# Kernel tuning notes

Hardware: AMD Instinct MI355X
Metric: run time of the kernel (lower is better)

The kernel has to match this reference:

```python
import jax, jax.numpy as jnp
import numpy as np

NUM_TABLES = 26
ROWS = 100000
EMB = 64
B = 4096
L = 32  # num_lookups per bag
BOT = [256, 512, 256, 64]
TOP = [EMB * (1 + NUM_TABLES), 512, 256, 1]


def _mlp_params(key, dims):
    params = []
    for i in range(len(dims) - 1):
        din, dout = dims[i], dims[i + 1]
        kw, kb, key = jax.random.split(key, 3)
        sw = np.sqrt(2.0 / (din + dout)).astype(np.float32)
        sb = np.sqrt(1.0 / dout).astype(np.float32)
        params.append((jax.random.normal(kw, (dout, din), jnp.float32) * sw,
                       jax.random.normal(kb, (dout,), jnp.float32) * sb))
    return params


def setup_inputs() -> dict:
    key = jax.random.key(0)
    k0, k1, k2, k3, k4 = jax.random.split(key, 5)
    inp = {}
    inp["x_dense"] = jax.random.normal(k0, (B, BOT[0]), jnp.float32)
    inp["x_indices"] = jax.random.randint(k1, (NUM_TABLES, B, L), 0, ROWS)
    bound = np.sqrt(1.0 / ROWS).astype(np.float32)
    inp["emb_tables"] = jax.random.uniform(k2, (NUM_TABLES, ROWS, EMB), jnp.float32, -bound, bound)
    for i, (w, b) in enumerate(_mlp_params(k3, BOT)):
        inp[f"bot_w{i}"] = w
        inp[f"bot_b{i}"] = b
    for i, (w, b) in enumerate(_mlp_params(k4, TOP)):
        inp[f"top_w{i}"] = w
        inp[f"top_b{i}"] = b
    return inp


def _forward(x_dense, x_indices, emb_tables, bot, top):
    # bottom MLP: Linear+ReLU per layer
    h = x_dense
    for w, b in bot:
        h = jax.nn.relu(h @ w.T + b)
    # multi-table EmbeddingBag(mode='sum'): gather rows then sum over bag dim
    # pooled: [T, B, E]
    pooled = jax.vmap(lambda tbl, idx: jnp.take(tbl, idx, axis=0).sum(axis=1))(emb_tables, x_indices)
    emb = jnp.transpose(pooled, (1, 0, 2)).reshape(x_dense.shape[0], -1)  # [B, T*E]
    z = jnp.concatenate([h, emb], axis=1)  # [B, E*(1+T)]
    # top MLP: ReLU on all but last, sigmoid on last
    n = len(top)
    for i, (w, b) in enumerate(top):
        z = z @ w.T + b
        z = jax.nn.sigmoid(z) if i == n - 1 else jax.nn.relu(z)
    return z


def reference(x_dense, x_indices, emb_tables,
              bot_w0, bot_b0, bot_w1, bot_b1, bot_w2, bot_b2,
              top_w0, top_b0, top_w1, top_b1, top_w2, top_b2):
    bot = [(bot_w0, bot_b0), (bot_w1, bot_b1), (bot_w2, bot_b2)]
    top = [(top_w0, top_b0), (top_w1, top_b1), (top_w2, top_b2)]
    return _forward(x_dense, x_indices, emb_tables, bot, top)
```

## Files before the change

kernel.cpp:

```cpp
#include <hip/hip_runtime.h>
#include <hip/hip_bf16.h>
#include <math.h>

typedef __attribute__((ext_vector_type(8))) short short8;
typedef __attribute__((ext_vector_type(4))) float f32x4;

#define NUM_TABLES 26
#define ROWS 100000
#define EMB 64
#define BATCH 4096
#define LOOKUPS 32
#define ZDIM 1728

#define CAST_BLOCKS 128
#define BOT_BLOCKS 256
#define EMBED_BLOCKS (NUM_TABLES * BATCH / 4)

__device__ __forceinline__ unsigned short f2bf(float f) {
  unsigned int u = __float_as_uint(f);
  u += 0x7FFFu + ((u >> 16) & 1u);
  return (unsigned short)(u >> 16);
}
__device__ __forceinline__ float bf2f(unsigned short h) {
  return __uint_as_float(((unsigned int)h) << 16);
}

__device__ __forceinline__ void gload16(const void* g, void* l) {
  __builtin_amdgcn_global_load_lds(
      (const __attribute__((address_space(1))) void*)g,
      (__attribute__((address_space(3))) void*)l, 16, 0, 0);
}

__device__ __forceinline__ short8 wfrag_f32(const float* __restrict__ W, int K,
                                            int colbase, int l, int kc) {
  const float* p = W + (size_t)(colbase + (l & 15)) * K + kc * 32 + ((l >> 4) << 3);
  float4 u = *(const float4*)p;
  float4 v = *(const float4*)(p + 4);
  short8 f;
  f[0] = (short)f2bf(u.x); f[1] = (short)f2bf(u.y);
  f[2] = (short)f2bf(u.z); f[3] = (short)f2bf(u.w);
  f[4] = (short)f2bf(v.x); f[5] = (short)f2bf(v.y);
  f[6] = (short)f2bf(v.z); f[7] = (short)f2bf(v.w);
  return f;
}

struct MegaArgs {
  const float* cast_s[2];
  unsigned short* cast_d[2];
  int cast_n4[2];
  int cast_total;
  const float* x_dense;
  const float* bw0; const float* bb0;
  const float* bw1; const float* bb1;
  const float* bw2; const float* bb2;
  const int* idx;
  const float* tables;
  unsigned short* z;
};

__global__ void mega(MegaArgs a) {
  __shared__ unsigned short xb[16][256];
  __shared__ unsigned short h0[16][512];

  if (blockIdx.x < CAST_BLOCKS) {
    for (int i = blockIdx.x * blockDim.x + threadIdx.x; i < a.cast_total;
         i += CAST_BLOCKS * blockDim.x) {
      int r = i;
      #pragma unroll
      for (int sg = 0; sg < 2; ++sg) {
        if (r < a.cast_n4[sg]) {
          float4 v = ((const float4*)a.cast_s[sg])[r];
          ushort4 o;
          o.x = f2bf(v.x); o.y = f2bf(v.y); o.z = f2bf(v.z); o.w = f2bf(v.w);
          ((ushort4*)a.cast_d[sg])[r] = o;
          break;
        }
        r -= a.cast_n4[sg];
      }
    }
    return;
  }

  if (blockIdx.x < CAST_BLOCKS + BOT_BLOCKS) {
    int b0 = (int)(blockIdx.x - CAST_BLOCKS) << 4;
    int w = threadIdx.x >> 6;
    int l = threadIdx.x & 63;

    #pragma unroll
    for (int i = 0; i < 4; ++i) {
      int flat = i * 256 + threadIdx.x;
      int row = flat >> 6;
      int c4 = flat & 63;
      float4 v = *(const float4*)(a.x_dense + (size_t)(b0 + row) * 256 + c4 * 4);
      int chunk = c4 >> 1;
      int scol = ((chunk ^ (row & 7)) << 3) | ((c4 & 1) << 2);
      ushort4 o;
      o.x = f2bf(v.x); o.y = f2bf(v.y); o.z = f2bf(v.z); o.w = f2bf(v.w);
      *(ushort4*)&xb[row][scol] = o;
    }
    __syncthreads();

    int arow = l & 15;
    int sA = arow & 7;
    const char* xbp = (const char*)&xb[0][0];
    const char* h0p = (const char*)&h0[0][0];

    f32x4 acc0[8];
    #pragma unroll
    for (int n = 0; n < 8; ++n) acc0[n] = (f32x4){0.f, 0.f, 0.f, 0.f};
    for (int kc = 0; kc < 8; ++kc) {
      int c = kc * 4 + (l >> 4);
      short8 av = *(const short8*)(xbp + arow * 512 + ((c ^ sA) << 4));
      #pragma unroll
      for (int n = 0; n < 8; ++n) {
        short8 bv = wfrag_f32(a.bw0, 256, w * 128 + n * 16, l, kc);
        acc0[n] = __builtin_amdgcn_mfma_f32_16x16x32_bf16(av, bv, acc0[n], 0, 0, 0);
      }
    }
    #pragma unroll
    for (int n = 0; n < 8; ++n) {
      int col = w * 128 + n * 16 + (l & 15);
      float bv = a.bb0[col];
      int chunk = col >> 3;
      #pragma unroll
      for (int r = 0; r < 4; ++r) {
        int row = ((l >> 4) << 2) + r;
        float val = acc0[n][r] + bv;
        val = val > 0.f ? val : 0.f;
        h0[row][((chunk ^ (row & 7)) << 3) | (col & 7)] = f2bf(val);
      }
    }
    __syncthreads();

    f32x4 acc1[4];
    #pragma unroll
    for (int n = 0; n < 4; ++n) acc1[n] = (f32x4){0.f, 0.f, 0.f, 0.f};
    for (int kc = 0; kc < 16; ++kc) {
      int c = kc * 4 + (l >> 4);
      short8 av = *(const short8*)(h0p + arow * 1024 + ((c ^ sA) << 4));
      #pragma unroll
      for (int n = 0; n < 4; ++n) {
        short8 bv = wfrag_f32(a.bw1, 512, w * 64 + n * 16, l, kc);
        acc1[n] = __builtin_amdgcn_mfma_f32_16x16x32_bf16(av, bv, acc1[n], 0, 0, 0);
      }
    }
    __syncthreads();
    #pragma unroll
    for (int n = 0; n < 4; ++n) {
      int col = w * 64 + n * 16 + (l & 15);
      float bv = a.bb1[col];
      int chunk = col >> 3;
      #pragma unroll
      for (int r = 0; r < 4; ++r) {
        int row = ((l >> 4) << 2) + r;
        float val = acc1[n][r] + bv;
        val = val > 0.f ? val : 0.f;
        xb[row][((chunk ^ (row & 7)) << 3) | (col & 7)] = f2bf(val);
      }
    }
    __syncthreads();

    f32x4 acc2 = (f32x4){0.f, 0.f, 0.f, 0.f};
    for (int kc = 0; kc < 8; ++kc) {
      int c = kc * 4 + (l >> 4);
      short8 av = *(const short8*)(xbp + arow * 512 + ((c ^ sA) << 4));
      short8 bv = wfrag_f32(a.bw2, 256, w * 16, l, kc);
      acc2 = __builtin_amdgcn_mfma_f32_16x16x32_bf16(av, bv, acc2, 0, 0, 0);
    }
    {
      int col = w * 16 + (l & 15);
      float bv = a.bb2[col];
      #pragma unroll
      for (int r = 0; r < 4; ++r) {
        int row = ((l >> 4) << 2) + r;
        float val = acc2[r] + bv;
        val = val > 0.f ? val : 0.f;
        a.z[(size_t)(b0 + row) * ZDIM + col] = f2bf(val);
      }
    }
    return;
  }

  int g = (int)(((blockIdx.x - CAST_BLOCKS - BOT_BLOCKS) << 2) + (threadIdx.x >> 6));
  int lane = threadIdx.x & 63;
  int t = g >> 12;
  int b = g & 4095;
  const int* ip = a.idx + ((size_t)t * BATCH + b) * LOOKUPS;
  int myidx = (lane < LOOKUPS) ? ip[lane] : 0;
  const float* tbl = a.tables + (size_t)t * ROWS * EMB;
  int grp = lane >> 4;
  int e4 = lane & 15;
  float4 acc = {0.f, 0.f, 0.f, 0.f};
  #pragma unroll
  for (int it = 0; it < 8; ++it) {
    int r = __shfl(myidx, it * 4 + grp, 64);
    float4 v = ((const float4*)(tbl + (size_t)r * EMB))[e4];
    acc.x += v.x; acc.y += v.y; acc.z += v.z; acc.w += v.w;
  }
  #pragma unroll
  for (int m = 16; m <= 32; m <<= 1) {
    acc.x += __shfl_xor(acc.x, m, 64);
    acc.y += __shfl_xor(acc.y, m, 64);
    acc.z += __shfl_xor(acc.z, m, 64);
    acc.w += __shfl_xor(acc.w, m, 64);
  }
  if (lane < 16) {
    ushort4 o;
    o.x = f2bf(acc.x); o.y = f2bf(acc.y); o.z = f2bf(acc.z); o.w = f2bf(acc.w);
    *(ushort4*)&a.z[(size_t)b * ZDIM + EMB + t * EMB + e4 * 4] = o;
  }
}

template<int ACT>
__global__ __launch_bounds__(256) void gemm64s(
    const unsigned short* __restrict__ A,
    const unsigned short* __restrict__ W,
    const float* __restrict__ bias,
    unsigned short* __restrict__ C,
    int M, int N, int K, int ldc) {
  __shared__ unsigned short lds[2][64][64];

  int t = threadIdx.x;
  int lane = t & 63;
  int wid = t >> 6;
  int wr = wid >> 1;
  int wc = wid & 1;

  int bid = (int)blockIdx.x;
  int q = (int)gridDim.x >> 3;
  int swz = (bid & 7) * q + (bid >> 3);

  int ntn = N >> 6;
  int tm = swz / ntn;
  int tn = swz - tm * ntn;

  int srow = lane >> 3;
  int schunk = (lane & 7) ^ (srow & 7);
  const unsigned short* Ap0 = A + (size_t)(tm * 64 + wid * 16 + srow) * K + schunk * 8;
  const unsigned short* Wp0 = W + (size_t)(tn * 64 + wid * 16 + srow) * K + schunk * 8;
  size_t rowK8 = (size_t)8 * K;

  f32x4 acc[2][2];
  #pragma unroll
  for (int m = 0; m < 2; ++m)
    #pragma unroll
    for (int n = 0; n < 2; ++n)
      acc[m][n] = (f32x4){0.f, 0.f, 0.f, 0.f};

  int ra = wr * 32 + (lane & 15);
  int rb = wc * 32 + (lane & 15);
  int cidx = lane >> 4;
  int sA = ra & 7, sB = rb & 7;

  for (int k0 = 0; k0 < K; k0 += 64) {
    #pragma unroll
    for (int j = 0; j < 2; ++j) {
      gload16(Ap0 + (size_t)k0 + j * rowK8, &lds[0][wid * 16 + j * 8][0]);
      gload16(Wp0 + (size_t)k0 + j * rowK8, &lds[1][wid * 16 + j * 8][0]);
    }
    __syncthreads();

    const char* bA = (const char*)&lds[0][0][0];
    const char* bB = (const char*)&lds[1][0][0];
    #pragma unroll
    for (int kc = 0; kc < 2; ++kc) {
      int c = kc * 4 + cidx;
      short8 a0 = *(const short8*)(bA + ra * 128 + ((c ^ sA) << 4));
      short8 a1 = *(const short8*)(bA + (ra + 16) * 128 + ((c ^ sA) << 4));
      short8 b0 = *(const short8*)(bB + rb * 128 + ((c ^ sB) << 4));
      short8 b1 = *(const short8*)(bB + (rb + 16) * 128 + ((c ^ sB) << 4));
      acc[0][0] = __builtin_amdgcn_mfma_f32_16x16x32_bf16(a0, b0, acc[0][0], 0, 0, 0);
      acc[0][1] = __builtin_amdgcn_mfma_f32_16x16x32_bf16(a0, b1, acc[0][1], 0, 0, 0);
      acc[1][0] = __builtin_amdgcn_mfma_f32_16x16x32_bf16(a1, b0, acc[1][0], 0, 0, 0);
      acc[1][1] = __builtin_amdgcn_mfma_f32_16x16x32_bf16(a1, b1, acc[1][1], 0, 0, 0);
    }
    __syncthreads();
  }

  #pragma unroll
  for (int m = 0; m < 2; ++m) {
    int drow = tm * 64 + wr * 32 + m * 16 + ((lane >> 4) << 2);
    #pragma unroll
    for (int n = 0; n < 2; ++n) {
      int dcol = tn * 64 + wc * 32 + n * 16 + (lane & 15);
      float bv = bias[dcol];
      #pragma unroll
      for (int r = 0; r < 4; ++r) {
        float v = acc[m][n][r] + bv;
        if (ACT == 1) v = v > 0.f ? v : 0.f;
        C[(size_t)(drow + r) * ldc + dcol] = f2bf(v);
      }
    }
  }
}

__global__ __launch_bounds__(256) void topfin256(
    const unsigned short* __restrict__ z1,
    const unsigned short* __restrict__ w1,
    const float* __restrict__ b1,
    const float* __restrict__ w2,
    const float* __restrict__ b2,
    float* __restrict__ out) {
  __shared__ float red[4][16];
  int l = threadIdx.x & 63;
  int w = threadIdx.x >> 6;
  int row0 = (int)blockIdx.x * 16;

  f32x4 acc[4];
  #pragma unroll
  for (int n = 0; n < 4; ++n) acc[n] = (f32x4){0.f, 0.f, 0.f, 0.f};

  const unsigned short* ap0 = z1 + (size_t)(row0 + (l & 15)) * 512 + ((l >> 4) << 3);
  const unsigned short* bp0 = w1 + (size_t)(w * 64 + (l & 15)) * 512 + ((l >> 4) << 3);
  #pragma unroll 4
  for (int kc = 0; kc < 16; ++kc) {
    short8 av = *(const short8*)(ap0 + kc * 32);
    #pragma unroll
    for (int n = 0; n < 4; ++n) {
      short8 bv = *(const short8*)(bp0 + (size_t)n * 16 * 512 + kc * 32);
      acc[n] = __builtin_amdgcn_mfma_f32_16x16x32_bf16(av, bv, acc[n], 0, 0, 0);
    }
  }

  float s0 = 0.f, s1 = 0.f, s2 = 0.f, s3 = 0.f;
  #pragma unroll
  for (int n = 0; n < 4; ++n) {
    int col = w * 64 + n * 16 + (l & 15);
    float bv = b1[col];
    float wv = w2[col];
    float v0 = acc[n][0] + bv; v0 = v0 > 0.f ? v0 : 0.f; s0 += v0 * wv;
    float v1 = acc[n][1] + bv; v1 = v1 > 0.f ? v1 : 0.f; s1 += v1 * wv;
    float v2 = acc[n][2] + bv; v2 = v2 > 0.f ? v2 : 0.f; s2 += v2 * wv;
    float v3 = acc[n][3] + bv; v3 = v3 > 0.f ? v3 : 0.f; s3 += v3 * wv;
  }
  #pragma unroll
  for (int m = 1; m <= 8; m <<= 1) {
    s0 += __shfl_xor(s0, m, 64);
    s1 += __shfl_xor(s1, m, 64);
    s2 += __shfl_xor(s2, m, 64);
    s3 += __shfl_xor(s3, m, 64);
  }
  if ((l & 15) == 0) {
    int rbase = (l >> 4) * 4;
    red[w][rbase + 0] = s0;
    red[w][rbase + 1] = s1;
    red[w][rbase + 2] = s2;
    red[w][rbase + 3] = s3;
  }
  __syncthreads();
  if (threadIdx.x < 16) {
    float s = red[0][threadIdx.x] + red[1][threadIdx.x] +
              red[2][threadIdx.x] + red[3][threadIdx.x];
    out[row0 + threadIdx.x] = 1.f / (1.f + expf(-(s + b2[0])));
  }
}

extern "C" void kernel_launch(void* const* d_in, const int* in_sizes, int n_in,
                              void* d_out, int out_size, void* d_ws, size_t ws_size,
                              hipStream_t stream) {
  const float* x_dense = (const float*)d_in[0];
  const int*   x_idx   = (const int*)d_in[1];
  const float* tables  = (const float*)d_in[2];
  const float* bw0 = (const float*)d_in[3];  const float* bb0 = (const float*)d_in[4];
  const float* bw1 = (const float*)d_in[5];  const float* bb1 = (const float*)d_in[6];
  const float* bw2 = (const float*)d_in[7];  const float* bb2 = (const float*)d_in[8];
  const float* tw0 = (const float*)d_in[9];  const float* tb0 = (const float*)d_in[10];
  const float* tw1 = (const float*)d_in[11]; const float* tb1 = (const float*)d_in[12];
  const float* tw2 = (const float*)d_in[13]; const float* tb2 = (const float*)d_in[14];
  float* out = (float*)d_out;

  char* ws = (char*)d_ws;
  size_t off = 0;
  auto alloc = [&](size_t bytes) { void* p = ws + off; off += (bytes + 255) & ~(size_t)255; return p; };
  unsigned short* tw0b = (unsigned short*)alloc((size_t)512 * ZDIM * 2);
  unsigned short* tw1b = (unsigned short*)alloc((size_t)256 * 512 * 2);
  unsigned short* z    = (unsigned short*)alloc((size_t)BATCH * ZDIM * 2);
  unsigned short* z1   = (unsigned short*)alloc((size_t)BATCH * 512 * 2);

  {
    MegaArgs a;
    a.cast_s[0] = tw0; a.cast_d[0] = tw0b; a.cast_n4[0] = 512 * ZDIM / 4;
    a.cast_s[1] = tw1; a.cast_d[1] = tw1b; a.cast_n4[1] = 256 * 512 / 4;
    a.cast_total = a.cast_n4[0] + a.cast_n4[1];
    a.x_dense = x_dense;
    a.bw0 = bw0; a.bb0 = bb0;
    a.bw1 = bw1; a.bb1 = bb1;
    a.bw2 = bw2; a.bb2 = bb2;
    a.idx = x_idx;
    a.tables = tables;
    a.z = z;
    mega<<<CAST_BLOCKS + BOT_BLOCKS + EMBED_BLOCKS, 256, 0, stream>>>(a);
  }

  gemm64s<1><<<512, 256, 0, stream>>>(z, tw0b, tb0, z1, BATCH, 512, ZDIM, 512);

  topfin256<<<BATCH / 16, 256, 0, stream>>>(z1, tw1b, tb1, tw2, tb2, out);
}
```

Before: 174.9 us.

## Split-K the top-layer-0 GEMM three ways and fuse the reduction into the final kernel

The 4096x512x1728 GEMM now runs as a 3-way split-K over 1536 blocks instead of 512, so more CUs stay busy. Each split writes fp32 partial sums to a workspace. The final kernel sums the three partials, adds bias and ReLU, converts to bf16 and stages the result in swizzled LDS before its MFMA loop. In exchange it writes and reads about 24 MB of fp32 partials instead of a 4 MB bf16 intermediate.

```diff
diff --git a/kernel.cpp b/kernel.cpp
--- a/kernel.cpp
+++ b/kernel.cpp
@@ -211,13 +211,10 @@
   }
 }
 
-template<int ACT>
-__global__ __launch_bounds__(256) void gemm64s(
+__global__ __launch_bounds__(256) void gemm_top0_sk(
     const unsigned short* __restrict__ A,
     const unsigned short* __restrict__ W,
-    const float* __restrict__ bias,
-    unsigned short* __restrict__ C,
-    int M, int N, int K, int ldc) {
+    float* __restrict__ z1p) {
   __shared__ unsigned short lds[2][64][64];
 
   int t = threadIdx.x;
@@ -227,18 +224,18 @@
   int wc = wid & 1;
 
   int bid = (int)blockIdx.x;
-  int q = (int)gridDim.x >> 3;
-  int swz = (bid & 7) * q + (bid >> 3);
-
-  int ntn = N >> 6;
-  int tm = swz / ntn;
-  int tn = swz - tm * ntn;
+  int swz = (bid & 7) * 192 + (bid >> 3);
+  int kh = swz / 512;
+  int tid = swz - kh * 512;
+  int tm = tid >> 3;
+  int tn = tid & 7;
+  int kstart = kh * 576;
 
   int srow = lane >> 3;
   int schunk = (lane & 7) ^ (srow & 7);
-  const unsigned short* Ap0 = A + (size_t)(tm * 64 + wid * 16 + srow) * K + schunk * 8;
-  const unsigned short* Wp0 = W + (size_t)(tn * 64 + wid * 16 + srow) * K + schunk * 8;
-  size_t rowK8 = (size_t)8 * K;
+  const unsigned short* Ap0 = A + (size_t)(tm * 64 + wid * 16 + srow) * ZDIM + schunk * 8;
+  const unsigned short* Wp0 = W + (size_t)(tn * 64 + wid * 16 + srow) * ZDIM + schunk * 8;
+  size_t rowK8 = (size_t)8 * ZDIM;
 
   f32x4 acc[2][2];
   #pragma unroll
@@ -252,7 +249,8 @@
   int cidx = lane >> 4;
   int sA = ra & 7, sB = rb & 7;
 
-  for (int k0 = 0; k0 < K; k0 += 64) {
+  for (int s = 0; s < 9; ++s) {
+    int k0 = kstart + s * 64;
     #pragma unroll
     for (int j = 0; j < 2; ++j) {
       gload16(Ap0 + (size_t)k0 + j * rowK8, &lds[0][wid * 16 + j * 8][0]);
@@ -277,44 +275,72 @@
     __syncthreads();
   }
 
+  float* Cp = z1p + (size_t)kh * BATCH * 512;
   #pragma unroll
   for (int m = 0; m < 2; ++m) {
     int drow = tm * 64 + wr * 32 + m * 16 + ((lane >> 4) << 2);
     #pragma unroll
     for (int n = 0; n < 2; ++n) {
       int dcol = tn * 64 + wc * 32 + n * 16 + (lane & 15);
-      float bv = bias[dcol];
-      #pragma unroll
-      for (int r = 0; r < 4; ++r) {
-        float v = acc[m][n][r] + bv;
-        if (ACT == 1) v = v > 0.f ? v : 0.f;
-        C[(size_t)(drow + r) * ldc + dcol] = f2bf(v);
-      }
+      #pragma unroll
+      for (int r = 0; r < 4; ++r)
+        Cp[(size_t)(drow + r) * 512 + dcol] = acc[m][n][r];
     }
   }
 }
 
 __global__ __launch_bounds__(256) void topfin256(
-    const unsigned short* __restrict__ z1,
+    const float* __restrict__ z1p,
+    const float* __restrict__ tb0,
     const unsigned short* __restrict__ w1,
-    const float* __restrict__ b1,
+    const float* __restrict__ tb1,
     const float* __restrict__ w2,
     const float* __restrict__ b2,
     float* __restrict__ out) {
+  __shared__ unsigned short zb[16][512];
   __shared__ float red[4][16];
   int l = threadIdx.x & 63;
   int w = threadIdx.x >> 6;
   int row0 = (int)blockIdx.x * 16;
 
+  const float* p0 = z1p;
+  const float* p1 = z1p + (size_t)BATCH * 512;
+  const float* p2 = z1p + (size_t)2 * BATCH * 512;
+
+  #pragma unroll
+  for (int i = 0; i < 8; ++i) {
+    int idx4 = i * 256 + threadIdx.x;
+    int row = idx4 >> 7;
+    int col = (idx4 & 127) * 4;
+    size_t gi = (size_t)(row0 + row) * 512 + col;
+    float4 v0 = *(const float4*)(p0 + gi);
+    float4 v1 = *(const float4*)(p1 + gi);
+    float4 v2 = *(const float4*)(p2 + gi);
+    float4 bb = *(const float4*)(tb0 + col);
+    float e0 = v0.x + v1.x + v2.x + bb.x; e0 = e0 > 0.f ? e0 : 0.f;
+    float e1 = v0.y + v1.y + v2.y + bb.y; e1 = e1 > 0.f ? e1 : 0.f;
+    float e2 = v0.z + v1.z + v2.z + bb.z; e2 = e2 > 0.f ? e2 : 0.f;
+    float e3 = v0.w + v1.w + v2.w + bb.w; e3 = e3 > 0.f ? e3 : 0.f;
+    ushort4 o;
+    o.x = f2bf(e0); o.y = f2bf(e1); o.z = f2bf(e2); o.w = f2bf(e3);
+    int chunk = col >> 3;
+    int scol = ((chunk ^ (row & 7)) << 3) | (col & 7);
+    *(ushort4*)&zb[row][scol] = o;
+  }
+  __syncthreads();
+
   f32x4 acc[4];
   #pragma unroll
   for (int n = 0; n < 4; ++n) acc[n] = (f32x4){0.f, 0.f, 0.f, 0.f};
 
-  const unsigned short* ap0 = z1 + (size_t)(row0 + (l & 15)) * 512 + ((l >> 4) << 3);
+  const char* zbp = (const char*)&zb[0][0];
+  int arow = l & 15;
+  int sA = arow & 7;
   const unsigned short* bp0 = w1 + (size_t)(w * 64 + (l & 15)) * 512 + ((l >> 4) << 3);
   #pragma unroll 4
   for (int kc = 0; kc < 16; ++kc) {
-    short8 av = *(const short8*)(ap0 + kc * 32);
+    int c = kc * 4 + (l >> 4);
+    short8 av = *(const short8*)(zbp + arow * 1024 + ((c ^ sA) << 4));
     #pragma unroll
     for (int n = 0; n < 4; ++n) {
       short8 bv = *(const short8*)(bp0 + (size_t)n * 16 * 512 + kc * 32);
@@ -326,7 +352,7 @@
   #pragma unroll
   for (int n = 0; n < 4; ++n) {
     int col = w * 64 + n * 16 + (l & 15);
-    float bv = b1[col];
+    float bv = tb1[col];
     float wv = w2[col];
     float v0 = acc[n][0] + bv; v0 = v0 > 0.f ? v0 : 0.f; s0 += v0 * wv;
     float v1 = acc[n][1] + bv; v1 = v1 > 0.f ? v1 : 0.f; s1 += v1 * wv;
@@ -375,7 +401,7 @@
   unsigned short* tw0b = (unsigned short*)alloc((size_t)512 * ZDIM * 2);
   unsigned short* tw1b = (unsigned short*)alloc((size_t)256 * 512 * 2);
   unsigned short* z    = (unsigned short*)alloc((size_t)BATCH * ZDIM * 2);
-  unsigned short* z1   = (unsigned short*)alloc((size_t)BATCH * 512 * 2);
+  float*          z1p  = (float*)alloc((size_t)3 * BATCH * 512 * 4);
 
   {
     MegaArgs a;
@@ -392,7 +418,7 @@
     mega<<<CAST_BLOCKS + BOT_BLOCKS + EMBED_BLOCKS, 256, 0, stream>>>(a);
   }
 
-  gemm64s<1><<<512, 256, 0, stream>>>(z, tw0b, tb0, z1, BATCH, 512, ZDIM, 512);
-
-  topfin256<<<BATCH / 16, 256, 0, stream>>>(z1, tw1b, tb1, tw2, tb2, out);
-}
+  gemm_top0_sk<<<1536, 256, 0, stream>>>(z, tw0b, z1p);
+
+  topfin256<<<BATCH / 16, 256, 0, stream>>>(z1p, tb0, tw1b, tb1, tw2, tb2, out);
+}
```

After: 179.6 us. 2.7% more time.
